# Kernel tuning notes

Hardware: AMD Instinct MI355X
Metric: run time of the kernel (lower is better)

## Reference

```python
import jax, jax.numpy as jnp
import numpy as np

B, T, E, WIN, OC, VOCAB = 256, 2048, 128, 5, 128, 50000


def setup_inputs() -> dict:
    key = jax.random.key(0)
    k1, k2, k3, k4, k5, k6 = jax.random.split(key, 6)
    return {
        "x": jax.random.randint(k1, (B, T), 0, VOCAB + 1, dtype=jnp.int32),
        "emb_table": jax.random.normal(k2, (VOCAB + 1, E), dtype=jnp.float32),
        "att_w": jax.random.normal(k3, (WIN, E), dtype=jnp.float32) * 0.05,
        "att_b": jax.random.normal(k4, (1,), dtype=jnp.float32),
        "cnn_w": jax.random.normal(k5, (OC, E), dtype=jnp.float32) * 0.05,
        "cnn_b": jax.random.normal(k6, (OC,), dtype=jnp.float32),
    }


def reference(x, emb_table, att_w, att_b, cnn_w, cnn_b):
    win = att_w.shape[0]
    pad = (win - 1) // 2
    embed = emb_table[x]                                   # [B, T, E]
    x_pad = jnp.pad(embed, ((0, 0), (pad, pad), (0, 0)))
    T_ = embed.shape[1]
    # Sliding-window dot product over full embed dim (the degenerate Conv2d)
    s = jnp.zeros(embed.shape[:2], dtype=embed.dtype)      # [B, T]
    for k in range(win):
        s = s + jnp.einsum('bte,e->bt', x_pad[:, k:k + T_, :], att_w[k])
    scores = jax.nn.sigmoid(s + att_b[0])                  # [B, T]
    gated = embed * scores[:, :, None]                     # [B, T, E]
    feat = jnp.tanh(jnp.einsum('bte,oe->bto', gated, cnn_w) + cnn_b)  # [B, T, OC]
    out = jnp.max(feat, axis=1)                            # [B, OC] (maxpool over seq)
    return out[:, :, None, None]                           # [B, OC, 1, 1]
```

## Files before the change

kernel.cpp:

```cpp
#include <hip/hip_runtime.h>
#include <hip/hip_bf16.h>
#include <math.h>

#define B_   256
#define T_   2048
#define E_   128
#define WIN_ 5
#define PAD_ 2
#define OC_  128
#define VOCAB_MAX 50000
#define VOCAB1 50001
#define TT   64
#define REAL_ROWS (TT + WIN_ - 1)
#define ROWS 80
#define ASTR 136
#define VROWS 64
#define BT   512

typedef __attribute__((ext_vector_type(8))) short short8;
typedef __attribute__((ext_vector_type(4))) float floatx4;
typedef __attribute__((ext_vector_type(4))) unsigned uintx4;

static __device__ __forceinline__ short f2bf(float f) {
    union { __hip_bfloat16 h; short s; } u;
    u.h = __float2bfloat16(f);
    return u.s;
}

__device__ __forceinline__ void atomicMaxFloat(float* addr, float v) {
    if (v >= 0.0f) atomicMax((int*)addr, __float_as_int(v));
    else           atomicMin((unsigned int*)addr, __float_as_uint(v));
}

__launch_bounds__(256, 4)
__global__ void build_tables(const float* __restrict__ emb,
                             const float* __restrict__ cnn_w,
                             const float* __restrict__ att_w,
                             short* __restrict__ D,
                             float* __restrict__ r,
                             float* __restrict__ out) {
    __shared__ short sh_a[VROWS * ASTR];
    __shared__ short sh_d[VROWS * ASTR];

    const int tid  = threadIdx.x;
    const int lane = tid & 63;
    const int w    = tid >> 6;
    const int l15  = lane & 15;
    const int quad = lane >> 4;
    const int v0   = blockIdx.x * VROWS;

    if (blockIdx.x < (B_ * OC_) / 256)
        out[blockIdx.x * 256 + tid] = -INFINITY;

    #pragma unroll
    for (int t = 0; t < 8; t++) {
        int i   = t * 256 + tid;
        int row = i >> 5, c4 = i & 31;
        int vr  = v0 + row; if (vr > VOCAB_MAX) vr = VOCAB_MAX;
        float4 v = *(const float4*)(emb + (size_t)vr * E_ + c4 * 4);
        short4 o; o.x = f2bf(v.x); o.y = f2bf(v.y); o.z = f2bf(v.z); o.w = f2bf(v.w);
        *(short4*)(&sh_a[row * ASTR + c4 * 4]) = o;
    }

    short8 Bf[2][4];
    #pragma unroll
    for (int j = 0; j < 2; j++)
        #pragma unroll
        for (int ks = 0; ks < 4; ks++) {
            const float4* p = (const float4*)(cnn_w + (size_t)(w * 32 + j * 16 + l15) * E_ + ks * 32 + quad * 8);
            float4 p0 = p[0], p1 = p[1];
            Bf[j][ks] = (short8){ f2bf(p0.x), f2bf(p0.y), f2bf(p0.z), f2bf(p0.w),
                                  f2bf(p1.x), f2bf(p1.y), f2bf(p1.z), f2bf(p1.w) };
        }

    short8 Ba[4];
    #pragma unroll
    for (int ks = 0; ks < 4; ks++) {
        short8 v = (short8){0,0,0,0,0,0,0,0};
        if (l15 < WIN_) {
            const float4* p = (const float4*)(att_w + (size_t)l15 * E_ + ks * 32 + quad * 8);
            float4 p0 = p[0], p1 = p[1];
            v = (short8){ f2bf(p0.x), f2bf(p0.y), f2bf(p0.z), f2bf(p0.w),
                          f2bf(p1.x), f2bf(p1.y), f2bf(p1.z), f2bf(p1.w) };
        }
        Ba[ks] = v;
    }
    __syncthreads();

    #pragma unroll
    for (int mt = 0; mt < 4; mt++) {
        short8 a[4];
        #pragma unroll
        for (int ks = 0; ks < 4; ks++)
            a[ks] = *(const short8*)(&sh_a[(mt * 16 + l15) * ASTR + ks * 32 + quad * 8]);
        #pragma unroll
        for (int j = 0; j < 2; j++) {
            floatx4 acc = (floatx4){0.f, 0.f, 0.f, 0.f};
            #pragma unroll
            for (int ks = 0; ks < 4; ks++)
                acc = __builtin_amdgcn_mfma_f32_16x16x32_bf16(a[ks], Bf[j][ks], acc, 0, 0, 0);
            #pragma unroll
            for (int rr = 0; rr < 4; rr++)
                sh_d[(mt * 16 + quad * 4 + rr) * ASTR + w * 32 + j * 16 + l15] = f2bf(acc[rr]);
        }
    }

    {
        short8 a[4];
        #pragma unroll
        for (int ks = 0; ks < 4; ks++)
            a[ks] = *(const short8*)(&sh_a[(w * 16 + l15) * ASTR + ks * 32 + quad * 8]);
        floatx4 acc = (floatx4){0.f, 0.f, 0.f, 0.f};
        #pragma unroll
        for (int ks = 0; ks < 4; ks++)
            acc = __builtin_amdgcn_mfma_f32_16x16x32_bf16(a[ks], Ba[ks], acc, 0, 0, 0);
        if (l15 < 8) {
            #pragma unroll
            for (int rr = 0; rr < 4; rr++) {
                int v = v0 + w * 16 + quad * 4 + rr;
                if (v <= VOCAB_MAX) r[(size_t)v * 8 + l15] = acc[rr];
            }
        }
    }
    __syncthreads();

    #pragma unroll
    for (int st = 0; st < 4; st++) {
        int i   = st * 256 + tid;
        int row = i >> 4, c = i & 15;
        int v   = v0 + row;
        if (v <= VOCAB_MAX)
            *(short8*)(D + (size_t)v * E_ + c * 8) =
                *(const short8*)(&sh_d[row * ASTR + c * 8]);
    }
}

__launch_bounds__(256, 4)
__global__ void score_max(const int* __restrict__ x,
                          const short* __restrict__ D,
                          const float* __restrict__ r,
                          const float* __restrict__ att_b_p,
                          const float* __restrict__ cnn_b,
                          float* __restrict__ out) {
    __shared__ int   sh_x[BT + 4];
    __shared__ float sh_rt[WIN_][BT + 8];
    __shared__ float sh_sc[BT];
    __shared__ float sh_red[4][128];

    const int tid  = threadIdx.x;
    const int lane = tid & 63;
    const int w    = tid >> 6;
    const int b    = blockIdx.y;
    const int t0   = blockIdx.x * BT;
    const int l15  = lane & 15;
    const int grp  = lane >> 4;

    for (int i = tid; i < BT + 4; i += 256) {
        int t = t0 + i - PAD_;
        int v = (t >= 0 && t < T_) ? x[b * T_ + t] : -1;
        sh_x[i] = v;
        float4 r03 = make_float4(0.f, 0.f, 0.f, 0.f);
        float  r4  = 0.f;
        if (v >= 0) {
            r03 = *(const float4*)(r + (size_t)v * 8);
            r4  = r[(size_t)v * 8 + 4];
        }
        sh_rt[0][i] = r03.x; sh_rt[1][i] = r03.y; sh_rt[2][i] = r03.z;
        sh_rt[3][i] = r03.w; sh_rt[4][i] = r4;
    }
    __syncthreads();

    const int base_t = w * 128;

    uintx4 uA[8];
    #pragma unroll
    for (int j = 0; j < 8; j++) {
        int tok = base_t + j * 4 + grp;
        int v   = sh_x[tok + PAD_];
        uA[j]   = *(const uintx4*)(D + (size_t)v * E_ + l15 * 8);
    }

    {
        const float attb = att_b_p[0];
        #pragma unroll
        for (int rep = 0; rep < 2; rep++) {
            int j = rep * 256 + tid;
            float s = attb;
            #pragma unroll
            for (int k = 0; k < WIN_; k++) s += sh_rt[k][j + k];
            sh_sc[j] = 1.0f / (1.0f + __expf(-s));
        }
    }
    __syncthreads();

    float mm[8];
    #pragma unroll
    for (int c = 0; c < 8; c++) mm[c] = -INFINITY;

    #pragma unroll
    for (int batch = 0; batch < 4; batch++) {
        uintx4 uB[8];
        if (batch < 3) {
            const int nstart = base_t + (batch + 1) * 32;
            #pragma unroll
            for (int j = 0; j < 8; j++) {
                int tok = nstart + j * 4 + grp;
                int v   = sh_x[tok + PAD_];
                uB[j]   = *(const uintx4*)(D + (size_t)v * E_ + l15 * 8);
            }
        }

        const int start = base_t + batch * 32;
        float sc8[8];
        #pragma unroll
        for (int j = 0; j < 8; j++) sc8[j] = sh_sc[start + j * 4 + grp];

        #pragma unroll
        for (int j = 0; j < 8; j++) {
            #pragma unroll
            for (int q = 0; q < 4; q++) {
                float lo = __uint_as_float(uA[j][q] << 16);
                float hi = __uint_as_float(uA[j][q] & 0xFFFF0000u);
                mm[q * 2]     = fmaxf(mm[q * 2],     sc8[j] * lo);
                mm[q * 2 + 1] = fmaxf(mm[q * 2 + 1], sc8[j] * hi);
            }
        }

        #pragma unroll
        for (int j = 0; j < 8; j++) uA[j] = uB[j];
    }

    #pragma unroll
    for (int c = 0; c < 8; c++) {
        mm[c] = fmaxf(mm[c], __shfl_xor(mm[c], 16));
        mm[c] = fmaxf(mm[c], __shfl_xor(mm[c], 32));
    }
    if (lane < 16) {
        #pragma unroll
        for (int c = 0; c < 8; c++) sh_red[w][l15 * 8 + c] = mm[c];
    }
    __syncthreads();
    if (tid < 128) {
        float m = fmaxf(fmaxf(sh_red[0][tid], sh_red[1][tid]),
                        fmaxf(sh_red[2][tid], sh_red[3][tid]));
        atomicMaxFloat(&out[b * OC_ + tid], tanhf(m + cnn_b[tid]));
    }
}

__global__ void prep_small(const float* __restrict__ cnn_w, const float* __restrict__ att_w,
                           short* __restrict__ wsw, short* __restrict__ wsatt) {
    int i = blockIdx.x * 256 + threadIdx.x;
    if (i < OC_ * E_)  wsw[i]   = f2bf(cnn_w[i]);
    if (i < WIN_ * E_) wsatt[i] = f2bf(att_w[i]);
}

__launch_bounds__(256, 4)
__global__ void fallback_main(const int* __restrict__ x,
                              const float* __restrict__ emb,
                              const float* __restrict__ att_b_p,
                              const short* __restrict__ wsw,
                              const short* __restrict__ wsatt,
                              const float* __restrict__ cnn_b,
                              float* __restrict__ out) {
    __shared__ short sh_a[ROWS * ASTR];
    __shared__ short sh_att[16 * ASTR];
    __shared__ float sh_r[ROWS * 8];
    __shared__ float sh_score[TT];
    __shared__ int   sh_idx[8 * ROWS];

    const int tid  = threadIdx.x;
    const int lane = tid & 63;
    const int w    = tid >> 6;
    const int b    = blockIdx.y;
    const int t0   = blockIdx.x * (8 * TT);
    const int l15  = lane & 15;
    const int quad = lane >> 4;
    const int rbase = tid >> 4;
    const int c     = tid & 15;

    for (int i = tid; i < 8 * ROWS; i += 256) {
        int tile = i / ROWS, row = i - tile * ROWS;
        int t = t0 + tile * TT + row - PAD_;
        sh_idx[i] = (row < REAL_ROWS && t >= 0 && t < T_) ? x[b * T_ + t] : -1;
    }
    {
        int o = tid >> 4, cc = tid & 15;
        short8 v = (short8){0,0,0,0,0,0,0,0};
        if (o < WIN_) v = *(const short8*)(wsatt + o * E_ + cc * 8);
        *(short8*)(&sh_att[o * ASTR + cc * 8]) = v;
    }
    short8 Bf[2][4];
    #pragma unroll
    for (int j = 0; j < 2; j++)
        #pragma unroll
        for (int ks = 0; ks < 4; ks++)
            Bf[j][ks] = *(const short8*)(wsw + (size_t)(w * 32 + j * 16 + l15) * E_ + ks * 32 + quad * 8);
    __syncthreads();

    short8 g[5];
    #pragma unroll
    for (int k = 0; k < 5; k++) {
        int idx = sh_idx[rbase + 16 * k];
        short8 v = (short8){0,0,0,0,0,0,0,0};
        if (idx >= 0) {
            const float4* p = (const float4*)(emb + (size_t)idx * E_ + c * 8);
            float4 p0 = p[0], p1 = p[1];
            v = (short8){ f2bf(p0.x), f2bf(p0.y), f2bf(p0.z), f2bf(p0.w),
                          f2bf(p1.x), f2bf(p1.y), f2bf(p1.z), f2bf(p1.w) };
        }
        g[k] = v;
    }
    #pragma unroll
    for (int k = 0; k < 5; k++)
        *(short8*)(&sh_a[(rbase + 16 * k) * ASTR + c * 8]) = g[k];
    __syncthreads();

    const float attb = att_b_p[0];
    float mm[2] = { -INFINITY, -INFINITY };

    for (int it = 0; it < 8; it++) {
        for (int mt = w; mt < 5; mt += 4) {
            floatx4 acc = (floatx4){0.f, 0.f, 0.f, 0.f};
            #pragma unroll
            for (int ks = 0; ks < 4; ks++) {
                short8 a  = *(const short8*)(&sh_a[(mt * 16 + l15) * ASTR + ks * 32 + quad * 8]);
                short8 bs = *(const short8*)(&sh_att[l15 * ASTR + ks * 32 + quad * 8]);
                acc = __builtin_amdgcn_mfma_f32_16x16x32_bf16(a, bs, acc, 0, 0, 0);
            }
            if (l15 < 8) {
                #pragma unroll
                for (int r = 0; r < 4; r++)
                    sh_r[(mt * 16 + quad * 4 + r) * 8 + l15] = acc[r];
            }
        }
        __syncthreads();

        if (it + 1 < 8) {
            const int* idxp = &sh_idx[(it + 1) * ROWS];
            #pragma unroll
            for (int k = 0; k < 5; k++) {
                int idx = idxp[rbase + 16 * k];
                short8 v = (short8){0,0,0,0,0,0,0,0};
                if (idx >= 0) {
                    const float4* p = (const float4*)(emb + (size_t)idx * E_ + c * 8);
                    float4 p0 = p[0], p1 = p[1];
                    v = (short8){ f2bf(p0.x), f2bf(p0.y), f2bf(p0.z), f2bf(p0.w),
                                  f2bf(p1.x), f2bf(p1.y), f2bf(p1.z), f2bf(p1.w) };
                }
                g[k] = v;
            }
        }

        if (tid < TT) {
            float s = attb;
            #pragma unroll
            for (int k = 0; k < WIN_; k++) s += sh_r[(tid + k) * 8 + k];
            sh_score[tid] = 1.0f / (1.0f + __expf(-s));
        }

        floatx4 acc[4][2];
        #pragma unroll
        for (int i = 0; i < 4; i++)
            #pragma unroll
            for (int j = 0; j < 2; j++) acc[i][j] = (floatx4){0.f, 0.f, 0.f, 0.f};
        #pragma unroll
        for (int ks = 0; ks < 4; ks++) {
            int ko = ks * 32 + quad * 8;
            #pragma unroll
            for (int i = 0; i < 4; i++) {
                short8 ai = *(const short8*)(&sh_a[(PAD_ + i * 16 + l15) * ASTR + ko]);
                acc[i][0] = __builtin_amdgcn_mfma_f32_16x16x32_bf16(ai, Bf[0][ks], acc[i][0], 0, 0, 0);
                acc[i][1] = __builtin_amdgcn_mfma_f32_16x16x32_bf16(ai, Bf[1][ks], acc[i][1], 0, 0, 0);
            }
        }
        __syncthreads();

        #pragma unroll
        for (int i = 0; i < 4; i++) {
            #pragma unroll
            for (int r = 0; r < 4; r++) {
                float sc = sh_score[i * 16 + quad * 4 + r];
                mm[0] = fmaxf(mm[0], sc * acc[i][0][r]);
                mm[1] = fmaxf(mm[1], sc * acc[i][1][r]);
            }
        }

        if (it + 1 < 8) {
            #pragma unroll
            for (int k = 0; k < 5; k++)
                *(short8*)(&sh_a[(rbase + 16 * k) * ASTR + c * 8]) = g[k];
            __syncthreads();
        }
    }

    #pragma unroll
    for (int j = 0; j < 2; j++) {
        float m = mm[j];
        m = fmaxf(m, __shfl_xor(m, 16));
        m = fmaxf(m, __shfl_xor(m, 32));
        if (lane < 16) {
            int o = w * 32 + j * 16 + lane;
            atomicMaxFloat(&out[b * OC_ + o], tanhf(m + cnn_b[o]));
        }
    }
}

extern "C" void kernel_launch(void* const* d_in, const int* in_sizes, int n_in,
                              void* d_out, int out_size, void* d_ws, size_t ws_size,
                              hipStream_t stream) {
    const int*   x     = (const int*)d_in[0];
    const float* emb   = (const float*)d_in[1];
    const float* att_w = (const float*)d_in[2];
    const float* att_b = (const float*)d_in[3];
    const float* cnn_w = (const float*)d_in[4];
    const float* cnn_b = (const float*)d_in[5];
    float* out = (float*)d_out;

    const size_t d_elems = (size_t)VOCAB1 * E_;
    const size_t r_elems = (size_t)VOCAB1 * 8;
    const size_t need = d_elems * 2 + r_elems * 4 + 64;

    if (ws_size >= need) {
        short* Dt = (short*)d_ws;
        float* rt = (float*)(Dt + d_elems);
        build_tables<<<(VOCAB1 + VROWS - 1) / VROWS, 256, 0, stream>>>(emb, cnn_w, att_w, Dt, rt, out);
        dim3 grid(T_ / BT, B_);
        score_max<<<grid, 256, 0, stream>>>(x, Dt, rt, att_b, cnn_b, out);
    } else {
        hipMemsetAsync(d_out, 0xFF, (size_t)B_ * OC_ * sizeof(float), stream);
        short* ws_w   = (short*)d_ws;
        short* ws_att = ws_w + OC_ * E_;
        prep_small<<<16, 256, 0, stream>>>(cnn_w, att_w, ws_w, ws_att);
        dim3 grid(T_ / (8 * TT), B_);
        fallback_main<<<grid, 256, 0, stream>>>(x, emb, att_b, ws_w, ws_att, cnn_b, out);
    }
}
```

Measured before the change: 110.5 us.

## Fuse table build and score-max into one persistent kernel with grid barrier

Merges the vocabulary table-building kernel and the score/max-pool kernel into a single launch of 1024 blocks. The first 782 blocks build the bf16 projected table and the attention-score table, then every block waits on an atomic-counter grid barrier before running the score and max phase. Token indices are prefetched before the barrier, and the score-phase shared buffers reuse the table-phase memory. The goal is to remove the second kernel launch and the gap between kernels. In exchange it adds a memset of the barrier counter and relies on all 1024 blocks being resident at once, which risks deadlock if occupancy falls short.

```diff
diff --git a/kernel.cpp b/kernel.cpp
--- a/kernel.cpp
+++ b/kernel.cpp
@@ -15,7 +15,9 @@
 #define ROWS 80
 #define ASTR 136
 #define VROWS 64
+#define NBLK_A ((VOCAB1 + VROWS - 1) / VROWS)
 #define BT   512
+#define NBLK 1024
 
 typedef __attribute__((ext_vector_type(8))) short short8;
 typedef __attribute__((ext_vector_type(4))) float floatx4;
@@ -33,140 +35,150 @@
 }
 
 __launch_bounds__(256, 4)
-__global__ void build_tables(const float* __restrict__ emb,
-                             const float* __restrict__ cnn_w,
-                             const float* __restrict__ att_w,
-                             short* __restrict__ D,
-                             float* __restrict__ r,
-                             float* __restrict__ out) {
-    __shared__ short sh_a[VROWS * ASTR];
-    __shared__ short sh_d[VROWS * ASTR];
+__global__ void fused_all(const int* __restrict__ x,
+                          const float* __restrict__ emb,
+                          const float* __restrict__ cnn_w,
+                          const float* __restrict__ att_w,
+                          const float* __restrict__ att_b_p,
+                          const float* __restrict__ cnn_b,
+                          short* __restrict__ D,
+                          float* __restrict__ r,
+                          unsigned* __restrict__ bar,
+                          float* __restrict__ out) {
+    __shared__ __align__(16) short sh_a[VROWS * ASTR];
+    __shared__ __align__(16) short sh_d[VROWS * ASTR];
+    __shared__ int sh_x[BT + 4];
 
     const int tid  = threadIdx.x;
     const int lane = tid & 63;
     const int w    = tid >> 6;
     const int l15  = lane & 15;
     const int quad = lane >> 4;
-    const int v0   = blockIdx.x * VROWS;
-
-    if (blockIdx.x < (B_ * OC_) / 256)
-        out[blockIdx.x * 256 + tid] = -INFINITY;
-
-    #pragma unroll
-    for (int t = 0; t < 8; t++) {
-        int i   = t * 256 + tid;
-        int row = i >> 5, c4 = i & 31;
-        int vr  = v0 + row; if (vr > VOCAB_MAX) vr = VOCAB_MAX;
-        float4 v = *(const float4*)(emb + (size_t)vr * E_ + c4 * 4);
-        short4 o; o.x = f2bf(v.x); o.y = f2bf(v.y); o.z = f2bf(v.z); o.w = f2bf(v.w);
-        *(short4*)(&sh_a[row * ASTR + c4 * 4]) = o;
-    }
-
-    short8 Bf[2][4];
-    #pragma unroll
-    for (int j = 0; j < 2; j++)
-        #pragma unroll
-        for (int ks = 0; ks < 4; ks++) {
-            const float4* p = (const float4*)(cnn_w + (size_t)(w * 32 + j * 16 + l15) * E_ + ks * 32 + quad * 8);
-            float4 p0 = p[0], p1 = p[1];
-            Bf[j][ks] = (short8){ f2bf(p0.x), f2bf(p0.y), f2bf(p0.z), f2bf(p0.w),
-                                  f2bf(p1.x), f2bf(p1.y), f2bf(p1.z), f2bf(p1.w) };
-        }
-
-    short8 Ba[4];
-    #pragma unroll
-    for (int ks = 0; ks < 4; ks++) {
-        short8 v = (short8){0,0,0,0,0,0,0,0};
-        if (l15 < WIN_) {
-            const float4* p = (const float4*)(att_w + (size_t)l15 * E_ + ks * 32 + quad * 8);
-            float4 p0 = p[0], p1 = p[1];
-            v = (short8){ f2bf(p0.x), f2bf(p0.y), f2bf(p0.z), f2bf(p0.w),
-                          f2bf(p1.x), f2bf(p1.y), f2bf(p1.z), f2bf(p1.w) };
-        }
-        Ba[ks] = v;
-    }
-    __syncthreads();
-
-    #pragma unroll
-    for (int mt = 0; mt < 4; mt++) {
-        short8 a[4];
-        #pragma unroll
-        for (int ks = 0; ks < 4; ks++)
-            a[ks] = *(const short8*)(&sh_a[(mt * 16 + l15) * ASTR + ks * 32 + quad * 8]);
-        #pragma unroll
-        for (int j = 0; j < 2; j++) {
-            floatx4 acc = (floatx4){0.f, 0.f, 0.f, 0.f};
-            #pragma unroll
-            for (int ks = 0; ks < 4; ks++)
-                acc = __builtin_amdgcn_mfma_f32_16x16x32_bf16(a[ks], Bf[j][ks], acc, 0, 0, 0);
-            #pragma unroll
-            for (int rr = 0; rr < 4; rr++)
-                sh_d[(mt * 16 + quad * 4 + rr) * ASTR + w * 32 + j * 16 + l15] = f2bf(acc[rr]);
-        }
-    }
-
-    {
-        short8 a[4];
-        #pragma unroll
-        for (int ks = 0; ks < 4; ks++)
-            a[ks] = *(const short8*)(&sh_a[(w * 16 + l15) * ASTR + ks * 32 + quad * 8]);
-        floatx4 acc = (floatx4){0.f, 0.f, 0.f, 0.f};
-        #pragma unroll
-        for (int ks = 0; ks < 4; ks++)
-            acc = __builtin_amdgcn_mfma_f32_16x16x32_bf16(a[ks], Ba[ks], acc, 0, 0, 0);
-        if (l15 < 8) {
-            #pragma unroll
-            for (int rr = 0; rr < 4; rr++) {
-                int v = v0 + w * 16 + quad * 4 + rr;
-                if (v <= VOCAB_MAX) r[(size_t)v * 8 + l15] = acc[rr];
-            }
-        }
-    }
-    __syncthreads();
-
-    #pragma unroll
-    for (int st = 0; st < 4; st++) {
-        int i   = st * 256 + tid;
-        int row = i >> 4, c = i & 15;
-        int v   = v0 + row;
-        if (v <= VOCAB_MAX)
-            *(short8*)(D + (size_t)v * E_ + c * 8) =
-                *(const short8*)(&sh_d[row * ASTR + c * 8]);
-    }
-}
-
-__launch_bounds__(256, 4)
-__global__ void score_max(const int* __restrict__ x,
-                          const short* __restrict__ D,
-                          const float* __restrict__ r,
-                          const float* __restrict__ att_b_p,
-                          const float* __restrict__ cnn_b,
-                          float* __restrict__ out) {
-    __shared__ int   sh_x[BT + 4];
-    __shared__ float sh_rt[WIN_][BT + 8];
-    __shared__ float sh_sc[BT];
-    __shared__ float sh_red[4][128];
-
-    const int tid  = threadIdx.x;
-    const int lane = tid & 63;
-    const int w    = tid >> 6;
-    const int b    = blockIdx.y;
-    const int t0   = blockIdx.x * BT;
-    const int l15  = lane & 15;
-    const int grp  = lane >> 4;
+    const int bid  = blockIdx.x;
+
+    const int b  = bid >> 2;
+    const int t0 = (bid & 3) * BT;
 
     for (int i = tid; i < BT + 4; i += 256) {
         int t = t0 + i - PAD_;
-        int v = (t >= 0 && t < T_) ? x[b * T_ + t] : -1;
-        sh_x[i] = v;
+        sh_x[i] = (t >= 0 && t < T_) ? x[b * T_ + t] : -1;
+    }
+
+    if (bid < NBLK_A) {
+        const int v0 = bid * VROWS;
+
+        if (bid < (B_ * OC_) / 256)
+            out[bid * 256 + tid] = -INFINITY;
+
+        #pragma unroll
+        for (int t = 0; t < 8; t++) {
+            int i   = t * 256 + tid;
+            int row = i >> 5, c4 = i & 31;
+            int vr  = v0 + row; if (vr > VOCAB_MAX) vr = VOCAB_MAX;
+            float4 v = *(const float4*)(emb + (size_t)vr * E_ + c4 * 4);
+            short4 o; o.x = f2bf(v.x); o.y = f2bf(v.y); o.z = f2bf(v.z); o.w = f2bf(v.w);
+            *(short4*)(&sh_a[row * ASTR + c4 * 4]) = o;
+        }
+
+        short8 Bf[2][4];
+        #pragma unroll
+        for (int j = 0; j < 2; j++)
+            #pragma unroll
+            for (int ks = 0; ks < 4; ks++) {
+                const float4* p = (const float4*)(cnn_w + (size_t)(w * 32 + j * 16 + l15) * E_ + ks * 32 + quad * 8);
+                float4 p0 = p[0], p1 = p[1];
+                Bf[j][ks] = (short8){ f2bf(p0.x), f2bf(p0.y), f2bf(p0.z), f2bf(p0.w),
+                                      f2bf(p1.x), f2bf(p1.y), f2bf(p1.z), f2bf(p1.w) };
+            }
+
+        short8 Ba[4];
+        #pragma unroll
+        for (int ks = 0; ks < 4; ks++) {
+            short8 v = (short8){0,0,0,0,0,0,0,0};
+            if (l15 < WIN_) {
+                const float4* p = (const float4*)(att_w + (size_t)l15 * E_ + ks * 32 + quad * 8);
+                float4 p0 = p[0], p1 = p[1];
+                v = (short8){ f2bf(p0.x), f2bf(p0.y), f2bf(p0.z), f2bf(p0.w),
+                              f2bf(p1.x), f2bf(p1.y), f2bf(p1.z), f2bf(p1.w) };
+            }
+            Ba[ks] = v;
+        }
+        __syncthreads();
+
+        #pragma unroll
+        for (int mt = 0; mt < 4; mt++) {
+            short8 a[4];
+            #pragma unroll
+            for (int ks = 0; ks < 4; ks++)
+                a[ks] = *(const short8*)(&sh_a[(mt * 16 + l15) * ASTR + ks * 32 + quad * 8]);
+            #pragma unroll
+            for (int j = 0; j < 2; j++) {
+                floatx4 acc = (floatx4){0.f, 0.f, 0.f, 0.f};
+                #pragma unroll
+                for (int ks = 0; ks < 4; ks++)
+                    acc = __builtin_amdgcn_mfma_f32_16x16x32_bf16(a[ks], Bf[j][ks], acc, 0, 0, 0);
+                #pragma unroll
+                for (int rr = 0; rr < 4; rr++)
+                    sh_d[(mt * 16 + quad * 4 + rr) * ASTR + w * 32 + j * 16 + l15] = f2bf(acc[rr]);
+            }
+        }
+
+        {
+            short8 a[4];
+            #pragma unroll
+            for (int ks = 0; ks < 4; ks++)
+                a[ks] = *(const short8*)(&sh_a[(w * 16 + l15) * ASTR + ks * 32 + quad * 8]);
+            floatx4 acc = (floatx4){0.f, 0.f, 0.f, 0.f};
+            #pragma unroll
+            for (int ks = 0; ks < 4; ks++)
+                acc = __builtin_amdgcn_mfma_f32_16x16x32_bf16(a[ks], Ba[ks], acc, 0, 0, 0);
+            if (l15 < 8) {
+                #pragma unroll
+                for (int rr = 0; rr < 4; rr++) {
+                    int v = v0 + w * 16 + quad * 4 + rr;
+                    if (v <= VOCAB_MAX) r[(size_t)v * 8 + l15] = acc[rr];
+                }
+            }
+        }
+        __syncthreads();
+
+        #pragma unroll
+        for (int st = 0; st < 4; st++) {
+            int i   = st * 256 + tid;
+            int row = i >> 4, c = i & 15;
+            int v   = v0 + row;
+            if (v <= VOCAB_MAX)
+                *(short8*)(D + (size_t)v * E_ + c * 8) =
+                    *(const short8*)(&sh_d[row * ASTR + c * 8]);
+        }
+    }
+
+    __syncthreads();
+    if (tid == 0) {
+        __threadfence();
+        __hip_atomic_fetch_add(bar, 1u, __ATOMIC_ACQ_REL, __HIP_MEMORY_SCOPE_AGENT);
+        while (__hip_atomic_load(bar, __ATOMIC_RELAXED, __HIP_MEMORY_SCOPE_AGENT) < NBLK)
+            __builtin_amdgcn_s_sleep(8);
+        __threadfence();
+    }
+    __syncthreads();
+
+    float* sh_rt = (float*)sh_a;
+    float* sh_sc = sh_rt + 5 * (BT + 8);
+    float* sh_red = sh_sc + BT;
+    const int grp = lane >> 4;
+
+    for (int i = tid; i < BT + 4; i += 256) {
+        int v = sh_x[i];
         float4 r03 = make_float4(0.f, 0.f, 0.f, 0.f);
         float  r4  = 0.f;
         if (v >= 0) {
             r03 = *(const float4*)(r + (size_t)v * 8);
             r4  = r[(size_t)v * 8 + 4];
         }
-        sh_rt[0][i] = r03.x; sh_rt[1][i] = r03.y; sh_rt[2][i] = r03.z;
-        sh_rt[3][i] = r03.w; sh_rt[4][i] = r4;
+        sh_rt[0 * (BT + 8) + i] = r03.x; sh_rt[1 * (BT + 8) + i] = r03.y;
+        sh_rt[2 * (BT + 8) + i] = r03.z; sh_rt[3 * (BT + 8) + i] = r03.w;
+        sh_rt[4 * (BT + 8) + i] = r4;
     }
     __syncthreads();
 
@@ -187,7 +199,7 @@
             int j = rep * 256 + tid;
             float s = attb;
             #pragma unroll
-            for (int k = 0; k < WIN_; k++) s += sh_rt[k][j + k];
+            for (int k = 0; k < WIN_; k++) s += sh_rt[k * (BT + 8) + j + k];
             sh_sc[j] = 1.0f / (1.0f + __expf(-s));
         }
     }
@@ -237,12 +249,12 @@
     }
     if (lane < 16) {
         #pragma unroll
-        for (int c = 0; c < 8; c++) sh_red[w][l15 * 8 + c] = mm[c];
+        for (int c = 0; c < 8; c++) sh_red[w * 128 + l15 * 8 + c] = mm[c];
     }
     __syncthreads();
     if (tid < 128) {
-        float m = fmaxf(fmaxf(sh_red[0][tid], sh_red[1][tid]),
-                        fmaxf(sh_red[2][tid], sh_red[3][tid]));
+        float m = fmaxf(fmaxf(sh_red[0 * 128 + tid], sh_red[1 * 128 + tid]),
+                        fmaxf(sh_red[2 * 128 + tid], sh_red[3 * 128 + tid]));
         atomicMaxFloat(&out[b * OC_ + tid], tanhf(m + cnn_b[tid]));
     }
 }
@@ -418,14 +430,14 @@
 
     const size_t d_elems = (size_t)VOCAB1 * E_;
     const size_t r_elems = (size_t)VOCAB1 * 8;
-    const size_t need = d_elems * 2 + r_elems * 4 + 64;
+    const size_t need = d_elems * 2 + r_elems * 4 + 128;
 
     if (ws_size >= need) {
-        short* Dt = (short*)d_ws;
-        float* rt = (float*)(Dt + d_elems);
-        build_tables<<<(VOCAB1 + VROWS - 1) / VROWS, 256, 0, stream>>>(emb, cnn_w, att_w, Dt, rt, out);
-        dim3 grid(T_ / BT, B_);
-        score_max<<<grid, 256, 0, stream>>>(x, Dt, rt, att_b, cnn_b, out);
+        short*    Dt  = (short*)d_ws;
+        float*    rt  = (float*)(Dt + d_elems);
+        unsigned* bar = (unsigned*)((char*)d_ws + d_elems * 2 + r_elems * 4);
+        hipMemsetAsync(bar, 0, 64, stream);
+        fused_all<<<NBLK, 256, 0, stream>>>(x, emb, cnn_w, att_w, att_b, cnn_b, Dt, rt, bar, out);
     } else {
         hipMemsetAsync(d_out, 0xFF, (size_t)B_ * OC_ * sizeof(float), stream);
         short* ws_w   = (short*)d_ws;
```

Result: slower. 235.4 us (+113.1%).
